# Performance work log

Hardware: AMD Instinct MI355X
Metric: run time of the kernel (lower is better)

## Reference

```python
import jax, jax.numpy as jnp
import numpy as np

NUM_CODES = 8192
CODE_DIM = 64
DECAY = 0.99
EPSILON = 1e-05
COMMITMENT_COST = 0.25


def setup_inputs() -> dict:
    key = jax.random.key(0)
    k1, k2, k3 = jax.random.split(key, 3)
    z = jax.random.normal(k1, (32768, CODE_DIM), dtype=jnp.float32)
    emb = jax.random.normal(k2, (NUM_CODES, CODE_DIM), dtype=jnp.float32)
    emb = emb / jnp.linalg.norm(emb, axis=1, keepdims=True)
    return {
        "z": z,
        "embedding": emb,
        "ema_cluster_size": jnp.zeros((NUM_CODES,), dtype=jnp.float32),
        "ema_embedding": emb.copy(),
    }


def reference(z, embedding, ema_cluster_size, ema_embedding):
    z_flat = z.reshape(-1, CODE_DIM)  # [N, D]
    # squared euclidean distances [N, K]
    distances = (
        jnp.sum(z_flat * z_flat, axis=1, keepdims=True)
        - 2.0 * (z_flat @ embedding.T)
        + jnp.sum(embedding * embedding, axis=1)
    )
    indices = jnp.argmin(distances, axis=1)  # [N] int
    z_q = embedding[indices]  # [N, D] gather

    # EMA buffer updates (training path), expressed as pure outputs.
    counts = jax.ops.segment_sum(
        jnp.ones_like(indices, dtype=z_flat.dtype), indices, num_segments=NUM_CODES
    )  # encodings.sum(0)
    dw = jax.ops.segment_sum(z_flat, indices, num_segments=NUM_CODES)  # encodings.T @ z_flat
    new_cluster_size = DECAY * ema_cluster_size + (1.0 - DECAY) * counts
    new_ema_embedding = DECAY * ema_embedding + (1.0 - DECAY) * dw
    n = jnp.sum(new_cluster_size)
    cluster_size = (new_cluster_size + EPSILON) / (n + NUM_CODES * EPSILON) * n
    new_embedding = new_ema_embedding / cluster_size[:, None]

    z_q_full = z_q.reshape(z.shape)
    z_q_st = z + jax.lax.stop_gradient(z_q_full - z)  # straight-through
    vq_loss = COMMITMENT_COST * jnp.mean(
        (jax.lax.stop_gradient(z_q_full) - z) ** 2
    )
    return (z_q_st, indices, vq_loss, new_embedding, new_cluster_size, new_ema_embedding)
```

## Files before the change

### kernel.cpp

```cpp
#include <hip/hip_runtime.h>

typedef _Float16 half8 __attribute__((ext_vector_type(8)));
typedef float f32x4 __attribute__((ext_vector_type(4)));

#define N_PTS   32768
#define DIMS    64
#define K_CODES 8192

#define OUT_ZQ      0
#define OUT_IDX     2097152
#define OUT_LOSS    2129920
#define OUT_NEWEMB  2129921
#define OUT_NCS     2654209
#define OUT_NEWEMA  2662401

#define SC_EHI      0
#define SC_ELO      262144
#define SC_ENSC     524288
#define SC_VAL1     532480
#define SC_IDX1     663552
#define SC_VAL2     794624
#define SC_FIXLIST  925696
#define SC_SORTED   929792
#define SC_OFFSETS  962560

#define WS_COUNTS   0
#define WS_CURSOR   8192
#define WS_LOSS     16384
#define WS_NSUM     16385
#define WS_FIXCNT   16386
#define WS_ZERO_BYTES (16388u * 4u)
#define WS_NCS      16388
#define WS_ENORM    24580
#define WS_IDX      32772
#define WS_DW       65540

#define MARGIN_SCALED 16.0f

__device__ inline void gld16(const void* g, void* l) {
    __builtin_amdgcn_global_load_lds((const __attribute__((address_space(1))) unsigned*)g,
                                     (__attribute__((address_space(3))) unsigned*)l, 16, 0, 0);
}
__device__ inline void gld4(const void* g, void* l) {
    __builtin_amdgcn_global_load_lds((const __attribute__((address_space(1))) unsigned*)g,
                                     (__attribute__((address_space(3))) unsigned*)l, 4, 0, 0);
}

__global__ __launch_bounds__(256) void esplit_kernel(const float* __restrict__ emb,
                                                     float4* __restrict__ ehi4,
                                                     float4* __restrict__ elo4,
                                                     float* __restrict__ ensc,
                                                     float* __restrict__ enorm) {
    int k = blockIdx.x * 256 + threadIdx.x;
    const float4* e4 = reinterpret_cast<const float4*>(emb + (size_t)k * DIMS);
    float vals[64];
    float sum = 0.0f;
#pragma unroll
    for (int i = 0; i < 16; ++i) {
        float4 v = e4[i];
        vals[i*4+0] = v.x; vals[i*4+1] = v.y; vals[i*4+2] = v.z; vals[i*4+3] = v.w;
        sum = fmaf(v.x, v.x, sum); sum = fmaf(v.y, v.y, sum);
        sum = fmaf(v.z, v.z, sum); sum = fmaf(v.w, v.w, sum);
    }
    enorm[k] = sum;
    ensc[k]  = 65536.0f * sum;
#pragma unroll
    for (int c = 0; c < 8; ++c) {
        union { _Float16 h[8]; float4 v; } uh, ul;
#pragma unroll
        for (int j = 0; j < 8; ++j) {
            float X = 256.0f * vals[c*8+j];
            _Float16 hh = (_Float16)X;
            uh.h[j] = hh;
            ul.h[j] = (_Float16)(X - (float)hh);
        }
        int cc = c ^ (k & 7);
        ehi4[(size_t)k*8 + cc] = uh.v;
        elo4[(size_t)k*8 + cc] = ul.v;
    }
}

__global__ __launch_bounds__(256, 2) void argmin_mfma(const float* __restrict__ z,
                                                      const char* __restrict__ ehi_g,
                                                      const char* __restrict__ elo_g,
                                                      const float* __restrict__ ensc_g,
                                                      float* __restrict__ val1,
                                                      int* __restrict__ idx1,
                                                      float* __restrict__ val2) {
    __shared__ __align__(16) char ebuf[2][2][8192];
    __shared__ float enb[2][64];

    const int tid = threadIdx.x;
    const int w   = tid >> 6;
    const int l   = tid & 63;
    const int l15 = l & 15;
    const int l4  = l >> 4;
    const int bid = blockIdx.x;
    const int rowbase = (bid >> 2) * 256 + w * 64;
    const int c0      = (bid & 3) * 2048;

    half8 ahi[4][2], alo[4][2];
#pragma unroll
    for (int s = 0; s < 4; ++s) {
        const float* zp = z + (size_t)(rowbase + s*16 + l15) * DIMS + l4 * 8;
#pragma unroll
        for (int ks = 0; ks < 2; ++ks) {
            float4 z0 = *reinterpret_cast<const float4*>(zp + ks*32);
            float4 z1 = *reinterpret_cast<const float4*>(zp + ks*32 + 4);
            float xv[8] = {z0.x, z0.y, z0.z, z0.w, z1.x, z1.y, z1.z, z1.w};
            half8 h, lo;
#pragma unroll
            for (int j = 0; j < 8; ++j) {
                float X = -512.0f * xv[j];
                _Float16 hh = (_Float16)X;
                h[j]  = hh;
                lo[j] = (_Float16)(X - (float)hh);
            }
            ahi[s][ks] = h; alo[s][ks] = lo;
        }
    }

    float b1[16], b2[16]; int i1[16];
#pragma unroll
    for (int r = 0; r < 16; ++r) { b1[r] = 3.4e38f; b2[r] = 3.4e38f; i1[r] = 0; }

    int rdoff[2];
#pragma unroll
    for (int ks = 0; ks < 2; ++ks)
        rdoff[ks] = l15 * 128 + (((ks*4 + l4) ^ (l15 & 7)) * 16);

    {
        const size_t gb = (size_t)c0 * 128;
        const char* sh = ehi_g + gb + tid*16;
        const char* sl = elo_g + gb + tid*16;
        char* dh = &ebuf[0][0][0] + w*1024;
        char* dl = &ebuf[0][1][0] + w*1024;
        gld16(sh,        dh);        gld16(sh + 4096, dh + 4096);
        gld16(sl,        dl);        gld16(sl + 4096, dl + 4096);
        if (w == 0) gld4(ensc_g + c0 + l, &enb[0][0]);
    }
    __syncthreads();

    int b = 0;
    for (int ch = 0; ch < 32; ++ch) {
        if (ch < 31) {
            const size_t gb = (size_t)(c0 + (ch+1)*64) * 128;
            const char* sh = ehi_g + gb + tid*16;
            const char* sl = elo_g + gb + tid*16;
            char* dh = &ebuf[b^1][0][0] + w*1024;
            char* dl = &ebuf[b^1][1][0] + w*1024;
            gld16(sh,        dh);        gld16(sh + 4096, dh + 4096);
            gld16(sl,        dl);        gld16(sl + 4096, dl + 4096);
            if (w == 0) gld4(ensc_g + c0 + (ch+1)*64 + l, &enb[b^1][0]);
        }
        const char* bhbase = &ebuf[b][0][0];
        const char* blbase = &ebuf[b][1][0];
#pragma unroll
        for (int t = 0; t < 4; ++t) {
            float en = enb[b][t*16 + l15];
            half8 bh[2], bl[2];
#pragma unroll
            for (int ks = 0; ks < 2; ++ks) {
                bh[ks] = *reinterpret_cast<const half8*>(bhbase + t*2048 + rdoff[ks]);
                bl[ks] = *reinterpret_cast<const half8*>(blbase + t*2048 + rdoff[ks]);
            }
            f32x4 acc[4];
#pragma unroll
            for (int s = 0; s < 4; ++s) acc[s] = (f32x4){en, en, en, en};
#pragma unroll
            for (int ks = 0; ks < 2; ++ks) {
#pragma unroll
                for (int s = 0; s < 4; ++s)
                    acc[s] = __builtin_amdgcn_mfma_f32_16x16x32_f16(ahi[s][ks], bh[ks], acc[s], 0, 0, 0);
#pragma unroll
                for (int s = 0; s < 4; ++s)
                    acc[s] = __builtin_amdgcn_mfma_f32_16x16x32_f16(ahi[s][ks], bl[ks], acc[s], 0, 0, 0);
#pragma unroll
                for (int s = 0; s < 4; ++s)
                    acc[s] = __builtin_amdgcn_mfma_f32_16x16x32_f16(alo[s][ks], bh[ks], acc[s], 0, 0, 0);
            }
            const int code = c0 + ch*64 + t*16 + l15;
#pragma unroll
            for (int s = 0; s < 4; ++s) {
#pragma unroll
                for (int j = 0; j < 4; ++j) {
                    const int r = s*4 + j;
                    float v = acc[s][j];
                    b2[r] = fminf(b2[r], fmaxf(b1[r], v));
                    bool c = v < b1[r];
                    b1[r] = c ? v : b1[r];
                    i1[r] = c ? code : i1[r];
                }
            }
        }
        __syncthreads();
        b ^= 1;
    }

#pragma unroll
    for (int m = 1; m < 16; m <<= 1) {
#pragma unroll
        for (int r = 0; r < 16; ++r) {
            float ob1 = __shfl_xor(b1[r], m, 64);
            int   oi1 = __shfl_xor(i1[r], m, 64);
            float ob2 = __shfl_xor(b2[r], m, 64);
            float nb2 = fminf(fminf(b2[r], ob2), fmaxf(b1[r], ob1));
            bool take = (ob1 < b1[r]) || (ob1 == b1[r] && oi1 < i1[r]);
            b1[r] = take ? ob1 : b1[r];
            i1[r] = take ? oi1 : i1[r];
            b2[r] = nb2;
        }
    }
    if (l15 == 0) {
        const int cs = bid & 3;
#pragma unroll
        for (int s = 0; s < 4; ++s)
#pragma unroll
            for (int j = 0; j < 4; ++j) {
                int row = rowbase + s*16 + l4*4 + j;
                int o = cs * N_PTS + row;
                val1[o] = b1[s*4+j];
                idx1[o] = i1[s*4+j];
                val2[o] = b2[s*4+j];
            }
    }
}

__global__ __launch_bounds__(256) void combine_kernel(const float* __restrict__ val1,
                                                      const int* __restrict__ idx1,
                                                      const float* __restrict__ val2,
                                                      int* __restrict__ ws_idx,
                                                      float* __restrict__ out_idxf,
                                                      int* __restrict__ fixcnt,
                                                      int* __restrict__ fixlist) {
    int row = blockIdx.x * 256 + threadIdx.x;
    float b1 = val1[row]; int i1 = idx1[row]; float b2 = val2[row];
#pragma unroll
    for (int c = 1; c < 4; ++c) {
        float ob1 = val1[c*N_PTS + row];
        int   oi1 = idx1[c*N_PTS + row];
        float ob2 = val2[c*N_PTS + row];
        float nb2 = fminf(fminf(b2, ob2), fmaxf(b1, ob1));
        if (ob1 < b1) { b1 = ob1; i1 = oi1; }
        b2 = nb2;
    }
    ws_idx[row]   = i1;
    out_idxf[row] = (float)i1;
    if (b2 - b1 < MARGIN_SCALED) {
        int p = atomicAdd(fixcnt, 1);
        if (p < 4096) fixlist[p] = row;
    }
}

__global__ __launch_bounds__(256) void fixup_kernel(const float* __restrict__ z,
                                                    const float* __restrict__ emb,
                                                    const float* __restrict__ enorm,
                                                    const int* __restrict__ fixcnt,
                                                    const int* __restrict__ fixlist,
                                                    int* __restrict__ ws_idx,
                                                    float* __restrict__ out_idxf) {
    __shared__ float zrow[64];
    __shared__ float rv[256];
    __shared__ int   ri[256];
    int cnt = *fixcnt; if (cnt > 4096) cnt = 4096;
    for (int g = blockIdx.x; g < cnt; g += 64) {
        int row = fixlist[g];
        __syncthreads();
        if (threadIdx.x < 64) zrow[threadIdx.x] = z[(size_t)row * DIMS + threadIdx.x];
        __syncthreads();
        float best = 3.4e38f; int bi = 0;
        for (int k = threadIdx.x; k < K_CODES; k += 256) {
            const float4* e4 = reinterpret_cast<const float4*>(emb + (size_t)k * DIMS);
            float s = 0.0f;
#pragma unroll
            for (int i = 0; i < 16; ++i) {
                float4 ev = e4[i];
                s = fmaf(zrow[i*4+0], ev.x, s);
                s = fmaf(zrow[i*4+1], ev.y, s);
                s = fmaf(zrow[i*4+2], ev.z, s);
                s = fmaf(zrow[i*4+3], ev.w, s);
            }
            float d = fmaf(-2.0f, s, enorm[k]);
            if (d < best) { best = d; bi = k; }
        }
        rv[threadIdx.x] = best; ri[threadIdx.x] = bi;
        __syncthreads();
        for (int off = 128; off > 0; off >>= 1) {
            if (threadIdx.x < off) {
                float ov = rv[threadIdx.x + off]; int oi = ri[threadIdx.x + off];
                if (ov < rv[threadIdx.x] || (ov == rv[threadIdx.x] && oi < ri[threadIdx.x])) {
                    rv[threadIdx.x] = ov; ri[threadIdx.x] = oi;
                }
            }
            __syncthreads();
        }
        if (threadIdx.x == 0) { ws_idx[row] = ri[0]; out_idxf[row] = (float)ri[0]; }
    }
}

__global__ __launch_bounds__(256) void hist_kernel(const int* __restrict__ idx,
                                                   float* __restrict__ counts) {
    int p = blockIdx.x * 256 + threadIdx.x;
    atomicAdd(&counts[idx[p]], 1.0f);
}

__global__ __launch_bounds__(256) void scan_kernel(const float* __restrict__ counts,
                                                   int* __restrict__ offsets) {
    __shared__ int excl[256];
    const int t = threadIdx.x;
    const int base = t * 32;
    int local[32];
    int s = 0;
#pragma unroll
    for (int i = 0; i < 32; ++i) { local[i] = s; s += (int)counts[base + i]; }
    __shared__ int tot[256];
    tot[t] = s;
    __syncthreads();
    if (t == 0) {
        int r = 0;
#pragma unroll 8
        for (int i = 0; i < 256; ++i) { excl[i] = r; r += tot[i]; }
    }
    __syncthreads();
    const int off = excl[t];
#pragma unroll
    for (int i = 0; i < 32; ++i) offsets[base + i] = off + local[i];
}

__global__ __launch_bounds__(256) void place_kernel(const int* __restrict__ idx,
                                                    const int* __restrict__ offsets,
                                                    int* __restrict__ cursor,
                                                    int* __restrict__ sorted) {
    int p = blockIdx.x * 256 + threadIdx.x;
    int k = idx[p];
    int pos = offsets[k] + atomicAdd(&cursor[k], 1);
    sorted[pos] = p;
}

__global__ __launch_bounds__(256) void dw_kernel(const float* __restrict__ z,
                                                 const int* __restrict__ sorted,
                                                 const int* __restrict__ offsets,
                                                 const float* __restrict__ counts,
                                                 float* __restrict__ dw) {
    const int w = threadIdx.x >> 6;
    const int lane = threadIdx.x & 63;
    const int k = blockIdx.x * 4 + w;
    const int start = offsets[k];
    const int cnt = (int)counts[k];
    float s = 0.0f;
    for (int i = 0; i < cnt; ++i) {
        int p = sorted[start + i];
        s += z[(size_t)p * DIMS + lane];
    }
    dw[(size_t)k * DIMS + lane] = s;
}

__global__ __launch_bounds__(256) void scatter_light(const float* __restrict__ z,
                                                     const float* __restrict__ emb,
                                                     const int* __restrict__ idx,
                                                     float* __restrict__ zq_out,
                                                     float* __restrict__ loss_accum) {
    const int tid = threadIdx.x;
    const int p = blockIdx.x * 64 + (tid >> 2);
    const int q = tid & 3;
    const int k = idx[p];

    const float4* zp = reinterpret_cast<const float4*>(z + (size_t)p * DIMS + q * 16);
    const float4* ep = reinterpret_cast<const float4*>(emb + (size_t)k * DIMS + q * 16);
    float4* op = reinterpret_cast<float4*>(zq_out + (size_t)p * DIMS + q * 16);

    float lsum = 0.0f;
#pragma unroll
    for (int i = 0; i < 4; ++i) {
        float4 zv = zp[i];
        float4 ev = ep[i];
        float4 t;
        t.x = ev.x - zv.x; t.y = ev.y - zv.y; t.z = ev.z - zv.z; t.w = ev.w - zv.w;
        lsum = fmaf(t.x, t.x, lsum); lsum = fmaf(t.y, t.y, lsum);
        lsum = fmaf(t.z, t.z, lsum); lsum = fmaf(t.w, t.w, lsum);
        float4 o;
        o.x = zv.x + t.x; o.y = zv.y + t.y; o.z = zv.z + t.z; o.w = zv.w + t.w;
        op[i] = o;
    }
#pragma unroll
    for (int o = 32; o > 0; o >>= 1) lsum += __shfl_down(lsum, o);
    if ((tid & 63) == 0) atomicAdd(loss_accum, lsum);
}

__global__ __launch_bounds__(256) void cs_kernel(const float* __restrict__ ema_cs,
                                                 const float* __restrict__ counts,
                                                 float* __restrict__ ncs_ws,
                                                 float* __restrict__ out_ncs,
                                                 float* __restrict__ n_accum) {
    const int k = blockIdx.x * 256 + threadIdx.x;
    float v = fmaf(0.99f, ema_cs[k], 0.01f * counts[k]);
    ncs_ws[k] = v;
    out_ncs[k] = v;
    float s = v;
#pragma unroll
    for (int o = 32; o > 0; o >>= 1) s += __shfl_down(s, o);
    __shared__ float ws_[4];
    if ((threadIdx.x & 63) == 0) ws_[threadIdx.x >> 6] = s;
    __syncthreads();
    if (threadIdx.x == 0) atomicAdd(n_accum, ws_[0] + ws_[1] + ws_[2] + ws_[3]);
}

__global__ __launch_bounds__(256) void final_kernel(const float* __restrict__ ema_emb,
                                                    const float* __restrict__ dw,
                                                    const float* __restrict__ ncs,
                                                    const float* __restrict__ n_ptr,
                                                    const float* __restrict__ loss_ptr,
                                                    float* __restrict__ out_newemb,
                                                    float* __restrict__ out_newema,
                                                    float* __restrict__ out_loss) {
    const int i = blockIdx.x * 256 + threadIdx.x;
    const int k = i >> 6;
    const float n = *n_ptr;
    const float cs = (ncs[k] + 1e-5f) / (n + (float)K_CODES * 1e-5f) * n;
    const float ne = fmaf(0.99f, ema_emb[i], 0.01f * dw[i]);
    out_newema[i] = ne;
    out_newemb[i] = ne / cs;
    if (i == 0) out_loss[0] = 0.25f * (loss_ptr[0] / 2097152.0f);
}

extern "C" void kernel_launch(void* const* d_in, const int* in_sizes, int n_in,
                              void* d_out, int out_size, void* d_ws, size_t ws_size,
                              hipStream_t stream) {
    const float* z       = (const float*)d_in[0];
    const float* emb     = (const float*)d_in[1];
    const float* ema_cs  = (const float*)d_in[2];
    const float* ema_emb = (const float*)d_in[3];
    float* out = (float*)d_out;
    float* ws  = (float*)d_ws;

    float* counts  = ws + WS_COUNTS;
    int*   cursor  = (int*)(ws + WS_CURSOR);
    float* loss    = ws + WS_LOSS;
    float* nsum    = ws + WS_NSUM;
    int*   fixcnt  = (int*)(ws + WS_FIXCNT);
    float* ncs     = ws + WS_NCS;
    float* enorm   = ws + WS_ENORM;
    int*   idx     = (int*)(ws + WS_IDX);
    float* dw      = ws + WS_DW;

    float* ehi     = out + SC_EHI;
    float* elo     = out + SC_ELO;
    float* ensc    = out + SC_ENSC;
    float* val1    = out + SC_VAL1;
    int*   idx1    = (int*)(out + SC_IDX1);
    float* val2    = out + SC_VAL2;
    int*   fixlist = (int*)(out + SC_FIXLIST);
    int*   sorted  = (int*)(out + SC_SORTED);
    int*   offsets = (int*)(out + SC_OFFSETS);

    hipMemsetAsync(d_ws, 0, WS_ZERO_BYTES, stream);

    esplit_kernel<<<K_CODES / 256, 256, 0, stream>>>(emb, (float4*)ehi, (float4*)elo, ensc, enorm);

    argmin_mfma<<<512, 256, 0, stream>>>(z, (const char*)ehi, (const char*)elo, ensc,
                                         val1, idx1, val2);

    combine_kernel<<<N_PTS / 256, 256, 0, stream>>>(val1, idx1, val2, idx, out + OUT_IDX,
                                                    fixcnt, fixlist);

    fixup_kernel<<<64, 256, 0, stream>>>(z, emb, enorm, fixcnt, fixlist, idx, out + OUT_IDX);

    hist_kernel<<<N_PTS / 256, 256, 0, stream>>>(idx, counts);

    scan_kernel<<<1, 256, 0, stream>>>(counts, offsets);

    place_kernel<<<N_PTS / 256, 256, 0, stream>>>(idx, offsets, cursor, sorted);

    dw_kernel<<<K_CODES / 4, 256, 0, stream>>>(z, sorted, offsets, counts, dw);

    scatter_light<<<N_PTS / 64, 256, 0, stream>>>(z, emb, idx, out + OUT_ZQ, loss);

    cs_kernel<<<K_CODES / 256, 256, 0, stream>>>(ema_cs, counts, ncs, out + OUT_NCS, nsum);

    final_kernel<<<(K_CODES * DIMS) / 256, 256, 0, stream>>>(ema_emb, dw, ncs, nsum, loss,
                                                             out + OUT_NEWEMB,
                                                             out + OUT_NEWEMA,
                                                             out + OUT_LOSS);
}
```

Measured before the change: 307.2 us.

## Split codebook 8 ways in argmin, fuse histogram and cluster-size into other kernels

```diff
diff --git a/kernel.cpp b/kernel.cpp
--- a/kernel.cpp
+++ b/kernel.cpp
@@ -18,11 +18,11 @@
 #define SC_ELO      262144
 #define SC_ENSC     524288
 #define SC_VAL1     532480
-#define SC_IDX1     663552
-#define SC_VAL2     794624
-#define SC_FIXLIST  925696
-#define SC_SORTED   929792
-#define SC_OFFSETS  962560
+#define SC_IDX1     794624
+#define SC_VAL2     1056768
+#define SC_FIXLIST  1318912
+#define SC_SORTED   1323008
+#define SC_OFFSETS  1355776
 
 #define WS_COUNTS   0
 #define WS_CURSOR   8192
@@ -80,7 +80,7 @@
     }
 }
 
-__global__ __launch_bounds__(256, 2) void argmin_mfma(const float* __restrict__ z,
+__global__ __launch_bounds__(256, 4) void argmin_mfma(const float* __restrict__ z,
                                                       const char* __restrict__ ehi_g,
                                                       const char* __restrict__ elo_g,
                                                       const float* __restrict__ ensc_g,
@@ -96,8 +96,8 @@
     const int l15 = l & 15;
     const int l4  = l >> 4;
     const int bid = blockIdx.x;
-    const int rowbase = (bid >> 2) * 256 + w * 64;
-    const int c0      = (bid & 3) * 2048;
+    const int rowbase = (bid >> 3) * 256 + w * 64;
+    const int c0      = (bid & 7) * 1024;
 
     half8 ahi[4][2], alo[4][2];
 #pragma unroll
@@ -142,8 +142,8 @@
     __syncthreads();
 
     int b = 0;
-    for (int ch = 0; ch < 32; ++ch) {
-        if (ch < 31) {
+    for (int ch = 0; ch < 16; ++ch) {
+        if (ch < 15) {
             const size_t gb = (size_t)(c0 + (ch+1)*64) * 128;
             const char* sh = ehi_g + gb + tid*16;
             const char* sl = elo_g + gb + tid*16;
@@ -158,6 +158,7 @@
 #pragma unroll
         for (int t = 0; t < 4; ++t) {
             float en = enb[b][t*16 + l15];
+            f32x4 envec = (f32x4){en, en, en, en};
             half8 bh[2], bl[2];
 #pragma unroll
             for (int ks = 0; ks < 2; ++ks) {
@@ -165,20 +166,27 @@
                 bl[ks] = *reinterpret_cast<const half8*>(blbase + t*2048 + rdoff[ks]);
             }
             f32x4 acc[4];
-#pragma unroll
-            for (int s = 0; s < 4; ++s) acc[s] = (f32x4){en, en, en, en};
-#pragma unroll
-            for (int ks = 0; ks < 2; ++ks) {
-#pragma unroll
-                for (int s = 0; s < 4; ++s)
-                    acc[s] = __builtin_amdgcn_mfma_f32_16x16x32_f16(ahi[s][ks], bh[ks], acc[s], 0, 0, 0);
-#pragma unroll
-                for (int s = 0; s < 4; ++s)
-                    acc[s] = __builtin_amdgcn_mfma_f32_16x16x32_f16(ahi[s][ks], bl[ks], acc[s], 0, 0, 0);
-#pragma unroll
-                for (int s = 0; s < 4; ++s)
-                    acc[s] = __builtin_amdgcn_mfma_f32_16x16x32_f16(alo[s][ks], bh[ks], acc[s], 0, 0, 0);
-            }
+            __builtin_amdgcn_s_setprio(1);
+#pragma unroll
+            for (int s = 0; s < 4; ++s)
+                acc[s] = __builtin_amdgcn_mfma_f32_16x16x32_f16(ahi[s][0], bh[0], envec, 0, 0, 0);
+#pragma unroll
+            for (int s = 0; s < 4; ++s)
+                acc[s] = __builtin_amdgcn_mfma_f32_16x16x32_f16(ahi[s][0], bl[0], acc[s], 0, 0, 0);
+#pragma unroll
+            for (int s = 0; s < 4; ++s)
+                acc[s] = __builtin_amdgcn_mfma_f32_16x16x32_f16(alo[s][0], bh[0], acc[s], 0, 0, 0);
+#pragma unroll
+            for (int s = 0; s < 4; ++s)
+                acc[s] = __builtin_amdgcn_mfma_f32_16x16x32_f16(ahi[s][1], bh[1], acc[s], 0, 0, 0);
+#pragma unroll
+            for (int s = 0; s < 4; ++s)
+                acc[s] = __builtin_amdgcn_mfma_f32_16x16x32_f16(ahi[s][1], bl[1], acc[s], 0, 0, 0);
+#pragma unroll
+            for (int s = 0; s < 4; ++s)
+                acc[s] = __builtin_amdgcn_mfma_f32_16x16x32_f16(alo[s][1], bh[1], acc[s], 0, 0, 0);
+            __builtin_amdgcn_s_setprio(0);
+
             const int code = c0 + ch*64 + t*16 + l15;
 #pragma unroll
             for (int s = 0; s < 4; ++s) {
@@ -212,7 +220,7 @@
         }
     }
     if (l15 == 0) {
-        const int cs = bid & 3;
+        const int cs = bid & 7;
 #pragma unroll
         for (int s = 0; s < 4; ++s)
 #pragma unroll
@@ -232,11 +240,12 @@
                                                       int* __restrict__ ws_idx,
                                                       float* __restrict__ out_idxf,
                                                       int* __restrict__ fixcnt,
-                                                      int* __restrict__ fixlist) {
+                                                      int* __restrict__ fixlist,
+                                                      float* __restrict__ counts) {
     int row = blockIdx.x * 256 + threadIdx.x;
     float b1 = val1[row]; int i1 = idx1[row]; float b2 = val2[row];
 #pragma unroll
-    for (int c = 1; c < 4; ++c) {
+    for (int c = 1; c < 8; ++c) {
         float ob1 = val1[c*N_PTS + row];
         int   oi1 = idx1[c*N_PTS + row];
         float ob2 = val2[c*N_PTS + row];
@@ -246,6 +255,7 @@
     }
     ws_idx[row]   = i1;
     out_idxf[row] = (float)i1;
+    atomicAdd(&counts[i1], 1.0f);
     if (b2 - b1 < MARGIN_SCALED) {
         int p = atomicAdd(fixcnt, 1);
         if (p < 4096) fixlist[p] = row;
@@ -258,7 +268,8 @@
                                                     const int* __restrict__ fixcnt,
                                                     const int* __restrict__ fixlist,
                                                     int* __restrict__ ws_idx,
-                                                    float* __restrict__ out_idxf) {
+                                                    float* __restrict__ out_idxf,
+                                                    float* __restrict__ counts) {
     __shared__ float zrow[64];
     __shared__ float rv[256];
     __shared__ int   ri[256];
@@ -294,37 +305,55 @@
             }
             __syncthreads();
         }
-        if (threadIdx.x == 0) { ws_idx[row] = ri[0]; out_idxf[row] = (float)ri[0]; }
-    }
-}
-
-__global__ __launch_bounds__(256) void hist_kernel(const int* __restrict__ idx,
-                                                   float* __restrict__ counts) {
-    int p = blockIdx.x * 256 + threadIdx.x;
-    atomicAdd(&counts[idx[p]], 1.0f);
-}
-
-__global__ __launch_bounds__(256) void scan_kernel(const float* __restrict__ counts,
-                                                   int* __restrict__ offsets) {
+        if (threadIdx.x == 0) {
+            int old = ws_idx[row];
+            if (ri[0] != old) {
+                atomicAdd(&counts[old], -1.0f);
+                atomicAdd(&counts[ri[0]], 1.0f);
+                ws_idx[row] = ri[0];
+                out_idxf[row] = (float)ri[0];
+            }
+        }
+    }
+}
+
+__global__ __launch_bounds__(256) void scan_cs_kernel(const float* __restrict__ ema_cs,
+                                                      const float* __restrict__ counts,
+                                                      float* __restrict__ ncs_ws,
+                                                      float* __restrict__ out_ncs,
+                                                      float* __restrict__ nsum,
+                                                      int* __restrict__ offsets) {
     __shared__ int excl[256];
+    __shared__ int tot[256];
+    __shared__ float fpart[256];
     const int t = threadIdx.x;
     const int base = t * 32;
-    int local[32];
-    int s = 0;
-#pragma unroll
-    for (int i = 0; i < 32; ++i) { local[i] = s; s += (int)counts[base + i]; }
-    __shared__ int tot[256];
-    tot[t] = s;
+    int loc[32];
+    int run = 0;
+    float fs = 0.0f;
+#pragma unroll
+    for (int i = 0; i < 32; ++i) {
+        float c = counts[base + i];
+        float v = fmaf(0.99f, ema_cs[base + i], 0.01f * c);
+        ncs_ws[base + i] = v;
+        out_ncs[base + i] = v;
+        fs += v;
+        loc[i] = run;
+        run += (int)c;
+    }
+    tot[t] = run;
+    fpart[t] = fs;
     __syncthreads();
     if (t == 0) {
         int r = 0;
-#pragma unroll 8
-        for (int i = 0; i < 256; ++i) { excl[i] = r; r += tot[i]; }
+        float f = 0.0f;
+        for (int i = 0; i < 256; ++i) { excl[i] = r; r += tot[i]; f += fpart[i]; }
+        nsum[0] = f;
     }
     __syncthreads();
     const int off = excl[t];
 #pragma unroll
-    for (int i = 0; i < 32; ++i) offsets[base + i] = off + local[i];
+    for (int i = 0; i < 32; ++i) offsets[base + i] = off + loc[i];
 }
 
 __global__ __launch_bounds__(256) void place_kernel(const int* __restrict__ idx,
@@ -385,24 +414,6 @@
 #pragma unroll
     for (int o = 32; o > 0; o >>= 1) lsum += __shfl_down(lsum, o);
     if ((tid & 63) == 0) atomicAdd(loss_accum, lsum);
-}
-
-__global__ __launch_bounds__(256) void cs_kernel(const float* __restrict__ ema_cs,
-                                                 const float* __restrict__ counts,
-                                                 float* __restrict__ ncs_ws,
-                                                 float* __restrict__ out_ncs,
-                                                 float* __restrict__ n_accum) {
-    const int k = blockIdx.x * 256 + threadIdx.x;
-    float v = fmaf(0.99f, ema_cs[k], 0.01f * counts[k]);
-    ncs_ws[k] = v;
-    out_ncs[k] = v;
-    float s = v;
-#pragma unroll
-    for (int o = 32; o > 0; o >>= 1) s += __shfl_down(s, o);
-    __shared__ float ws_[4];
-    if ((threadIdx.x & 63) == 0) ws_[threadIdx.x >> 6] = s;
-    __syncthreads();
-    if (threadIdx.x == 0) atomicAdd(n_accum, ws_[0] + ws_[1] + ws_[2] + ws_[3]);
 }
 
 __global__ __launch_bounds__(256) void final_kernel(const float* __restrict__ ema_emb,
@@ -457,25 +468,22 @@
 
     esplit_kernel<<<K_CODES / 256, 256, 0, stream>>>(emb, (float4*)ehi, (float4*)elo, ensc, enorm);
 
-    argmin_mfma<<<512, 256, 0, stream>>>(z, (const char*)ehi, (const char*)elo, ensc,
-                                         val1, idx1, val2);
+    argmin_mfma<<<1024, 256, 0, stream>>>(z, (const char*)ehi, (const char*)elo, ensc,
+                                          val1, idx1, val2);
 
     combine_kernel<<<N_PTS / 256, 256, 0, stream>>>(val1, idx1, val2, idx, out + OUT_IDX,
-                                                    fixcnt, fixlist);
-
-    fixup_kernel<<<64, 256, 0, stream>>>(z, emb, enorm, fixcnt, fixlist, idx, out + OUT_IDX);
-
-    hist_kernel<<<N_PTS / 256, 256, 0, stream>>>(idx, counts);
-
-    scan_kernel<<<1, 256, 0, stream>>>(counts, offsets);
+                                                    fixcnt, fixlist, counts);
+
+    fixup_kernel<<<64, 256, 0, stream>>>(z, emb, enorm, fixcnt, fixlist, idx, out + OUT_IDX,
+                                         counts);
+
+    scan_cs_kernel<<<1, 256, 0, stream>>>(ema_cs, counts, ncs, out + OUT_NCS, nsum, offsets);
 
     place_kernel<<<N_PTS / 256, 256, 0, stream>>>(idx, offsets, cursor, sorted);
 
     dw_kernel<<<K_CODES / 4, 256, 0, stream>>>(z, sorted, offsets, counts, dw);
 
     scatter_light<<<N_PTS / 64, 256, 0, stream>>>(z, emb, idx, out + OUT_ZQ, loss);
-
-    cs_kernel<<<K_CODES / 256, 256, 0, stream>>>(ema_cs, counts, ncs, out + OUT_NCS, nsum);
 
     final_kernel<<<(K_CODES * DIMS) / 256, 256, 0, stream>>>(ema_emb, dw, ncs, nsum, loss,
                                                              out + OUT_NEWEMB,
```

After: 761.3 us. 2.48x slower.
